# Kernel tuning notes

Hardware: AMD Instinct MI355X
Metric: run time of the kernel (lower is better)

## Reference

```python
import jax, jax.numpy as jnp
import numpy as np

IN_CH, OUT_CH, K, STRIDE = 128, 256, 3, 1

def setup_inputs() -> dict:
    key = jax.random.key(0)
    kx, kw = jax.random.split(key)
    x = jax.random.normal(kx, (32, IN_CH, 56, 56), dtype=jnp.float32)
    # xavier_uniform: bound = sqrt(6 / (fan_in + fan_out)), fans include receptive field
    fan_in = IN_CH * K * K
    fan_out = OUT_CH * K * K
    bound = float(np.sqrt(6.0 / (fan_in + fan_out)))
    weight = jax.random.uniform(kw, (OUT_CH, IN_CH, K, K), dtype=jnp.float32,
                                minval=-bound, maxval=bound)
    bias = jnp.zeros((OUT_CH,), dtype=jnp.float32)
    return {"x": x, "weight": weight, "bias": bias}

def reference(x, weight, bias):
    # VALID (no-padding) conv, stride STRIDE, NCHW layout, OIHW kernel
    out = jax.lax.conv_general_dilated(
        x, weight,
        window_strides=(STRIDE, STRIDE),
        padding="VALID",
        dimension_numbers=("NCHW", "OIHW", "NCHW"))
    return out + bias[None, :, None, None]
```

## Files before the change

### kernel.cpp

```cpp
#include <hip/hip_runtime.h>
#include <hip/hip_bf16.h>
#include <stdint.h>

#define NB    32
#define CIN   128
#define HIN   56
#define HW    (HIN*HIN)
#define OCH   256
#define OHW   54
#define SPB   (OHW*OHW)
#define KSZ   (CIN*9)
#define BM    256
#define BN    192
#define BK    32
#define NKS   (KSZ/BK)
#define TOTC  (NB*SPB)
#define NT    486
#define GRAN  ((BM+BN)*4)

typedef __attribute__((ext_vector_type(8))) short bf16x8;
typedef __attribute__((ext_vector_type(4))) float f32x4;

typedef __attribute__((address_space(1))) const uint32_t g_u32;
typedef __attribute__((address_space(3))) uint32_t l_u32;
static __device__ __forceinline__ void gl_lds16(const void* g, void* l) {
    __builtin_amdgcn_global_load_lds((g_u32*)g, (l_u32*)l, 16, 0, 0);
}

__global__ void xpose_cast(const float* __restrict__ x, __hip_bfloat16* __restrict__ xt) {
    __shared__ float tile[32][33];
    const int hw0 = blockIdx.x * 32;
    const int c0  = blockIdx.y * 32;
    const int n   = blockIdx.z;
    const int tx = threadIdx.x, ty = threadIdx.y;
    const float* xp = x + ((size_t)n*CIN + c0)*HW + hw0;
    #pragma unroll
    for (int i = ty; i < 32; i += 8)
        tile[i][tx] = xp[(size_t)i*HW + tx];
    __syncthreads();
    const int t = ty*32 + tx;
    const int hwl = t >> 3, q = t & 7;
    ushort4 v;
    v.x = __bfloat16_as_ushort(__float2bfloat16(tile[q*4+0][hwl]));
    v.y = __bfloat16_as_ushort(__float2bfloat16(tile[q*4+1][hwl]));
    v.z = __bfloat16_as_ushort(__float2bfloat16(tile[q*4+2][hwl]));
    v.w = __bfloat16_as_ushort(__float2bfloat16(tile[q*4+3][hwl]));
    __hip_bfloat16* op = xt + ((size_t)n*HW + hw0 + hwl)*CIN + c0 + q*4;
    *(ushort4*)op = v;
}

__global__ void wcast(const float* __restrict__ w, __hip_bfloat16* __restrict__ wt) {
    int tid = blockIdx.x*256 + threadIdx.x;
    if (tid >= OCH*KSZ) return;
    int oc = tid / KSZ, r = tid % KSZ;
    int pos = r >> 7, ic = r & 127;
    wt[tid] = __float2bfloat16(w[((size_t)(oc*CIN + ic))*9 + pos]);
}

__global__ __launch_bounds__(512, 2)
void conv_mfma(const __hip_bfloat16* __restrict__ xt,
               const __hip_bfloat16* __restrict__ wt,
               const float* __restrict__ bias,
               float* __restrict__ out) {
    __shared__ uint4 smem[3*GRAN];

    const int t = threadIdx.x;
    const int orig = blockIdx.x;
    const int xcd = orig & 7;
    const int tile = (xcd < 6 ? xcd*61 : 6*61 + (xcd-6)*60) + (orig >> 3);

    const int lane = t & 63, wid = t >> 6;
    const int wm = wid >> 2, wn = wid & 3;
    const int lr = lane & 15, lq = lane >> 4;

    const __hip_bfloat16* aptr[2];
    const __hip_bfloat16* bptr[2];
    #pragma unroll
    for (int i = 0; i < 2; ++i) {
        int q = i*512 + t;
        int row = q >> 2, j = q & 3;
        int ls = j ^ ((row >> 1) & 3);
        aptr[i] = wt + (size_t)row*KSZ + ls*8;
        int br = q & 1023;
        (void)br;
    }
    {
    }
    const __hip_bfloat16* bsrc0;
    const __hip_bfloat16* bsrc1;
    {
        int q0 = t;
        int r0 = q0 >> 2, j0 = q0 & 3, l0 = j0 ^ ((r0 >> 1) & 3);
        int c0 = tile*BN + r0;
        int n0 = c0 / SPB, rem0 = c0 - n0*SPB;
        bsrc0 = xt + ((size_t)(n0*HIN + rem0/OHW)*HIN + rem0%OHW)*CIN + l0*8;
        int q1 = 512 + (t & 255);
        int r1 = q1 >> 2, j1 = q1 & 3, l1 = j1 ^ ((r1 >> 1) & 3);
        int c1 = tile*BN + r1;
        int n1 = c1 / SPB, rem1 = c1 - n1*SPB;
        bsrc1 = xt + ((size_t)(n1*HIN + rem1/OHW)*HIN + rem1%OHW)*CIN + l1*8;
    }

    auto issueT = [&](int ks) {
        uint4* dst = smem + (ks % 3)*GRAN;
        const int aoff = ks*BK;
        const int pos = ks >> 2;
        const int kh = pos / 3, kw = pos - kh*3;
        const int boff = (kh*HIN + kw)*CIN + (ks & 3)*32;
        gl_lds16(aptr[0] + aoff, dst + t);
        gl_lds16(aptr[1] + aoff, dst + 512 + t);
        gl_lds16(bsrc0 + boff, dst + 1024 + t);
        if (t < 256) gl_lds16(bsrc1 + boff, dst + 1536 + t);
    };

    int ao[8], bo[3];
    #pragma unroll
    for (int mi = 0; mi < 8; ++mi) {
        int ra = wm*128 + mi*16 + lr;
        ao[mi] = ra*4 + (lq ^ ((ra >> 1) & 3));
    }
    #pragma unroll
    for (int ni = 0; ni < 3; ++ni) {
        int rb = wn*48 + ni*16 + lr;
        bo[ni] = 1024 + rb*4 + (lq ^ ((rb >> 1) & 3));
    }

    f32x4 acc[8][3];
    #pragma unroll
    for (int i = 0; i < 8; ++i)
        #pragma unroll
        for (int j = 0; j < 3; ++j)
            acc[i][j] = (f32x4){0.f, 0.f, 0.f, 0.f};

    #define MFMA_BF16 __builtin_amdgcn_mfma_f32_16x16x32_bf16
    #define VM_OWN() do { \
        if (wid < 4) asm volatile("s_waitcnt vmcnt(4)" ::: "memory"); \
        else         asm volatile("s_waitcnt vmcnt(3)" ::: "memory"); } while (0)

    issueT(0); issueT(1);
    VM_OWN();
    __builtin_amdgcn_s_barrier();
    __builtin_amdgcn_sched_barrier(0);

    for (int ks = 0; ks < NKS; ++ks) {
        const uint4* buf = smem + (ks % 3)*GRAN;
        bf16x8 a0[4], a1[4], b[3];
        #pragma unroll
        for (int mi = 0; mi < 4; ++mi) a0[mi] = *(bf16x8*)&buf[ao[mi]];
        #pragma unroll
        for (int ni = 0; ni < 3; ++ni) b[ni]  = *(bf16x8*)&buf[bo[ni]];
        if (ks + 2 < NKS) issueT(ks + 2);
        #pragma unroll
        for (int mi = 0; mi < 4; ++mi) a1[mi] = *(bf16x8*)&buf[ao[4 + mi]];

        asm volatile("s_waitcnt lgkmcnt(4)" ::: "memory");
        __builtin_amdgcn_sched_barrier(0);
        __builtin_amdgcn_s_setprio(1);
        #pragma unroll
        for (int mi = 0; mi < 4; ++mi)
            #pragma unroll
            for (int ni = 0; ni < 3; ++ni)
                acc[mi][ni] = MFMA_BF16(a0[mi], b[ni], acc[mi][ni], 0, 0, 0);
        __builtin_amdgcn_s_setprio(0);

        asm volatile("s_waitcnt lgkmcnt(0)" ::: "memory");
        __builtin_amdgcn_sched_barrier(0);
        __builtin_amdgcn_s_setprio(1);
        #pragma unroll
        for (int mi = 0; mi < 4; ++mi)
            #pragma unroll
            for (int ni = 0; ni < 3; ++ni)
                acc[4+mi][ni] = MFMA_BF16(a1[mi], b[ni], acc[4+mi][ni], 0, 0, 0);
        __builtin_amdgcn_s_setprio(0);

        if (ks + 1 < NKS) {
            if (ks + 2 < NKS) VM_OWN();
            else              asm volatile("s_waitcnt vmcnt(0)" ::: "memory");
            __builtin_amdgcn_s_barrier();
            __builtin_amdgcn_sched_barrier(0);
        }
    }

    __syncthreads();

    float (*eps)[196] = (float (*)[196])smem;
    const int cl4 = (t % 48) * 4;
    const int rsub = t / 48;
    const int colg = tile*BN + cl4;
    const int nn = colg / SPB;
    const int sp = colg - nn*SPB;
    #pragma unroll
    for (int h = 0; h < 4; ++h) {
        if (wm == (h >> 1)) {
            const int mib = (h & 1) * 4;
            #pragma unroll
            for (int ii = 0; ii < 4; ++ii) {
                int rl = ii*16 + lq*4;
                #pragma unroll
                for (int ni = 0; ni < 3; ++ni) {
                    int cl = wn*48 + ni*16 + lr;
                    #pragma unroll
                    for (int r = 0; r < 4; ++r)
                        eps[rl + r][cl] = acc[mib + ii][ni][r];
                }
            }
        }
        __syncthreads();
        if (t < 384) {
            #pragma unroll
            for (int pass = 0; pass < 8; ++pass) {
                int rl = pass*8 + rsub;
                int rg = h*64 + rl;
                f32x4 v = *(f32x4*)&eps[rl][cl4];
                v = v + bias[rg];
                *(f32x4*)&out[((size_t)nn*OCH + rg)*SPB + sp] = v;
            }
        }
        __syncthreads();
    }
}

__global__ void conv_naive(const float* __restrict__ x, const float* __restrict__ w,
                           const float* __restrict__ bias, float* __restrict__ out) {
    size_t tid = (size_t)blockIdx.x*256 + threadIdx.x;
    const size_t total = (size_t)NB*OCH*SPB;
    if (tid >= total) return;
    int col = (int)(tid % SPB);
    int oc  = (int)((tid / SPB) % OCH);
    int n   = (int)(tid / ((size_t)SPB*OCH));
    int oh = col / OHW, ow = col % OHW;
    float s = bias[oc];
    for (int ic = 0; ic < CIN; ++ic)
        #pragma unroll
        for (int kh = 0; kh < 3; ++kh)
            #pragma unroll
            for (int kw = 0; kw < 3; ++kw)
                s += x[((size_t)(n*CIN+ic)*HIN + oh+kh)*HIN + ow+kw]
                   * w[((size_t)(oc*CIN+ic)*3 + kh)*3 + kw];
    out[tid] = s;
}

extern "C" void kernel_launch(void* const* d_in, const int* in_sizes, int n_in,
                              void* d_out, int out_size, void* d_ws, size_t ws_size,
                              hipStream_t stream) {
    const float* x    = (const float*)d_in[0];
    const float* w    = (const float*)d_in[1];
    const float* bias = (const float*)d_in[2];
    float* out = (float*)d_out;

    const size_t xt_bytes = (size_t)NB*HW*CIN*sizeof(__hip_bfloat16);
    const size_t wt_bytes = (size_t)OCH*KSZ*sizeof(__hip_bfloat16);

    if (ws_size >= xt_bytes + wt_bytes) {
        __hip_bfloat16* xt  = (__hip_bfloat16*)d_ws;
        __hip_bfloat16* wtp = (__hip_bfloat16*)((char*)d_ws + xt_bytes);
        hipLaunchKernelGGL(xpose_cast, dim3(HW/32, CIN/32, NB), dim3(32, 8), 0, stream, x, xt);
        hipLaunchKernelGGL(wcast, dim3((OCH*KSZ + 255)/256), dim3(256), 0, stream, w, wtp);
        hipLaunchKernelGGL(conv_mfma, dim3(NT), dim3(512), 0, stream, xt, wtp, bias, out);
    } else {
        size_t total = (size_t)NB*OCH*SPB;
        hipLaunchKernelGGL(conv_naive, dim3((unsigned)((total + 255)/256)), dim3(256), 0, stream,
                           x, w, bias, out);
    }
}
```

Measured before the change: 85.82 us.

## Double K tile to 64 with double-buffered LDS and fewer barriers

Raises the K step from 32 to 64 and replaces the three-stage LDS ring with two larger buffers. It switches the LDS swizzle to an 8-chunk XOR pattern and runs two MFMA sub-steps per stage. This halves the number of block barriers and global-to-LDS issue rounds per output tile. In exchange the prefetch is now only one stage ahead and waits on vmcnt(0) every iteration, so memory latency may be less well hidden, and LDS use grows to about 114KB per block.

```diff
diff --git a/kernel.cpp b/kernel.cpp
--- a/kernel.cpp
+++ b/kernel.cpp
@@ -12,11 +12,11 @@
 #define KSZ   (CIN*9)
 #define BM    256
 #define BN    192
-#define BK    32
+#define BK    64
 #define NKS   (KSZ/BK)
 #define TOTC  (NB*SPB)
 #define NT    486
-#define GRAN  ((BM+BN)*4)
+#define GRAN  ((BM+BN)*8)
 
 typedef __attribute__((ext_vector_type(8))) short bf16x8;
 typedef __attribute__((ext_vector_type(4))) float f32x4;
@@ -62,7 +62,7 @@
                const __hip_bfloat16* __restrict__ wt,
                const float* __restrict__ bias,
                float* __restrict__ out) {
-    __shared__ uint4 smem[3*GRAN];
+    __shared__ uint4 smem[2*GRAN];
 
     const int t = threadIdx.x;
     const int orig = blockIdx.x;
@@ -73,56 +73,48 @@
     const int wm = wid >> 2, wn = wid & 3;
     const int lr = lane & 15, lq = lane >> 4;
 
-    const __hip_bfloat16* aptr[2];
-    const __hip_bfloat16* bptr[2];
-    #pragma unroll
-    for (int i = 0; i < 2; ++i) {
+    const __hip_bfloat16* aptr[4];
+    #pragma unroll
+    for (int i = 0; i < 4; ++i) {
         int q = i*512 + t;
-        int row = q >> 2, j = q & 3;
-        int ls = j ^ ((row >> 1) & 3);
+        int row = q >> 3, j = q & 7;
+        int ls = j ^ (row & 7);
         aptr[i] = wt + (size_t)row*KSZ + ls*8;
-        int br = q & 1023;
-        (void)br;
-    }
-    {
-    }
-    const __hip_bfloat16* bsrc0;
-    const __hip_bfloat16* bsrc1;
-    {
-        int q0 = t;
-        int r0 = q0 >> 2, j0 = q0 & 3, l0 = j0 ^ ((r0 >> 1) & 3);
-        int c0 = tile*BN + r0;
-        int n0 = c0 / SPB, rem0 = c0 - n0*SPB;
-        bsrc0 = xt + ((size_t)(n0*HIN + rem0/OHW)*HIN + rem0%OHW)*CIN + l0*8;
-        int q1 = 512 + (t & 255);
-        int r1 = q1 >> 2, j1 = q1 & 3, l1 = j1 ^ ((r1 >> 1) & 3);
-        int c1 = tile*BN + r1;
-        int n1 = c1 / SPB, rem1 = c1 - n1*SPB;
-        bsrc1 = xt + ((size_t)(n1*HIN + rem1/OHW)*HIN + rem1%OHW)*CIN + l1*8;
+    }
+    const __hip_bfloat16* bptr[3];
+    #pragma unroll
+    for (int i = 0; i < 3; ++i) {
+        int q = i*512 + t;
+        int row = q >> 3, j = q & 7;
+        int ls = j ^ (row & 7);
+        int colg = tile*BN + row;
+        int n = colg / SPB, rem = colg - n*SPB;
+        int oh = rem / OHW, ow = rem - oh*OHW;
+        bptr[i] = xt + ((size_t)(n*HIN + oh)*HIN + ow)*CIN + ls*8;
     }
 
     auto issueT = [&](int ks) {
-        uint4* dst = smem + (ks % 3)*GRAN;
+        uint4* dst = smem + (ks & 1)*GRAN;
         const int aoff = ks*BK;
-        const int pos = ks >> 2;
+        const int pos = ks >> 1;
         const int kh = pos / 3, kw = pos - kh*3;
-        const int boff = (kh*HIN + kw)*CIN + (ks & 3)*32;
-        gl_lds16(aptr[0] + aoff, dst + t);
-        gl_lds16(aptr[1] + aoff, dst + 512 + t);
-        gl_lds16(bsrc0 + boff, dst + 1024 + t);
-        if (t < 256) gl_lds16(bsrc1 + boff, dst + 1536 + t);
+        const int boff = (kh*HIN + kw)*CIN + (ks & 1)*64;
+        #pragma unroll
+        for (int i = 0; i < 4; ++i) gl_lds16(aptr[i] + aoff, dst + i*512 + t);
+        #pragma unroll
+        for (int i = 0; i < 3; ++i) gl_lds16(bptr[i] + boff, dst + 2048 + i*512 + t);
     };
 
     int ao[8], bo[3];
     #pragma unroll
     for (int mi = 0; mi < 8; ++mi) {
         int ra = wm*128 + mi*16 + lr;
-        ao[mi] = ra*4 + (lq ^ ((ra >> 1) & 3));
+        ao[mi] = ra*8 + (lq ^ (ra & 7));
     }
     #pragma unroll
     for (int ni = 0; ni < 3; ++ni) {
         int rb = wn*48 + ni*16 + lr;
-        bo[ni] = 1024 + rb*4 + (lq ^ ((rb >> 1) & 3));
+        bo[ni] = 2048 + rb*8 + (lq ^ (rb & 7));
     }
 
     f32x4 acc[8][3];
@@ -133,49 +125,55 @@
             acc[i][j] = (f32x4){0.f, 0.f, 0.f, 0.f};
 
     #define MFMA_BF16 __builtin_amdgcn_mfma_f32_16x16x32_bf16
-    #define VM_OWN() do { \
-        if (wid < 4) asm volatile("s_waitcnt vmcnt(4)" ::: "memory"); \
-        else         asm volatile("s_waitcnt vmcnt(3)" ::: "memory"); } while (0)
-
-    issueT(0); issueT(1);
-    VM_OWN();
+    #define MFMA12(AARR, MIB, BARR) \
+        __builtin_amdgcn_s_setprio(1); \
+        _Pragma("unroll") \
+        for (int ii = 0; ii < 4; ++ii) \
+            _Pragma("unroll") \
+            for (int ni = 0; ni < 3; ++ni) \
+                acc[(MIB)+ii][ni] = MFMA_BF16(AARR[ii], BARR[ni], acc[(MIB)+ii][ni], 0, 0, 0); \
+        __builtin_amdgcn_s_setprio(0);
+
+    issueT(0);
+    asm volatile("s_waitcnt vmcnt(0)" ::: "memory");
     __builtin_amdgcn_s_barrier();
     __builtin_amdgcn_sched_barrier(0);
 
     for (int ks = 0; ks < NKS; ++ks) {
-        const uint4* buf = smem + (ks % 3)*GRAN;
-        bf16x8 a0[4], a1[4], b[3];
-        #pragma unroll
-        for (int mi = 0; mi < 4; ++mi) a0[mi] = *(bf16x8*)&buf[ao[mi]];
-        #pragma unroll
-        for (int ni = 0; ni < 3; ++ni) b[ni]  = *(bf16x8*)&buf[bo[ni]];
-        if (ks + 2 < NKS) issueT(ks + 2);
-        #pragma unroll
-        for (int mi = 0; mi < 4; ++mi) a1[mi] = *(bf16x8*)&buf[ao[4 + mi]];
+        const uint4* buf = smem + (ks & 1)*GRAN;
+        bf16x8 a[4], a2[4], b[3];
+
+        #pragma unroll
+        for (int mi = 0; mi < 4; ++mi) a[mi] = *(bf16x8*)&buf[ao[mi]];
+        #pragma unroll
+        for (int ni = 0; ni < 3; ++ni) b[ni] = *(bf16x8*)&buf[bo[ni]];
+        if (ks + 1 < NKS) issueT(ks + 1);
+        #pragma unroll
+        for (int mi = 0; mi < 4; ++mi) a2[mi] = *(bf16x8*)&buf[ao[4 + mi]];
 
         asm volatile("s_waitcnt lgkmcnt(4)" ::: "memory");
         __builtin_amdgcn_sched_barrier(0);
-        __builtin_amdgcn_s_setprio(1);
-        #pragma unroll
-        for (int mi = 0; mi < 4; ++mi)
-            #pragma unroll
-            for (int ni = 0; ni < 3; ++ni)
-                acc[mi][ni] = MFMA_BF16(a0[mi], b[ni], acc[mi][ni], 0, 0, 0);
-        __builtin_amdgcn_s_setprio(0);
-
+        MFMA12(a, 0, b)
         asm volatile("s_waitcnt lgkmcnt(0)" ::: "memory");
         __builtin_amdgcn_sched_barrier(0);
-        __builtin_amdgcn_s_setprio(1);
-        #pragma unroll
-        for (int mi = 0; mi < 4; ++mi)
-            #pragma unroll
-            for (int ni = 0; ni < 3; ++ni)
-                acc[4+mi][ni] = MFMA_BF16(a1[mi], b[ni], acc[4+mi][ni], 0, 0, 0);
-        __builtin_amdgcn_s_setprio(0);
+        MFMA12(a2, 4, b)
+
+        #pragma unroll
+        for (int mi = 0; mi < 4; ++mi) a[mi] = *(bf16x8*)&buf[ao[mi] ^ 4];
+        #pragma unroll
+        for (int ni = 0; ni < 3; ++ni) b[ni] = *(bf16x8*)&buf[bo[ni] ^ 4];
+        #pragma unroll
+        for (int mi = 0; mi < 4; ++mi) a2[mi] = *(bf16x8*)&buf[ao[4 + mi] ^ 4];
+
+        asm volatile("s_waitcnt lgkmcnt(4)" ::: "memory");
+        __builtin_amdgcn_sched_barrier(0);
+        MFMA12(a, 0, b)
+        asm volatile("s_waitcnt lgkmcnt(0)" ::: "memory");
+        __builtin_amdgcn_sched_barrier(0);
+        MFMA12(a2, 4, b)
 
         if (ks + 1 < NKS) {
-            if (ks + 2 < NKS) VM_OWN();
-            else              asm volatile("s_waitcnt vmcnt(0)" ::: "memory");
+            asm volatile("s_waitcnt vmcnt(0)" ::: "memory");
             __builtin_amdgcn_s_barrier();
             __builtin_amdgcn_sched_barrier(0);
         }
```

Result: faster. 82.73 us (-3.6%).
